# Performance work log

Hardware: AMD Instinct MI355X
Metric: run time of the kernel (lower is better)

The kernel has to match this reference:

```python
import jax, jax.numpy as jnp
import numpy as np

N, E, IN, H, D = 50000, 800000, 256, 4, 32
NEG_SLOPE = 0.2


def setup_inputs() -> dict:
    key = jax.random.key(0)
    ks = jax.random.split(key, 11)
    feat = jax.random.normal(ks[0], (N, IN), jnp.float32)
    src = jax.random.randint(ks[1], (E,), 0, N, jnp.int32)
    dst = jax.random.randint(ks[2], (E,), 0, N, jnp.int32)
    # ppmi in [1, 10) so log(log(ppmi)) path is non-trivial
    ppmi = 1.0 + 9.0 * jax.random.uniform(ks[3], (E,), jnp.float32)
    eps_src = jax.random.normal(ks[4], (N, H, 1), jnp.float32)
    eps_dst = jax.random.normal(ks[5], (N, H, 1), jnp.float32)
    W = jax.random.normal(ks[6], (IN, H * D), jnp.float32) * (1.0 / np.sqrt(IN))
    mu_src = jax.random.normal(ks[7], (1, H, D), jnp.float32) * 0.02
    mu_dst = jax.random.normal(ks[8], (1, H, D), jnp.float32) * 0.02
    lam_src = jax.random.normal(ks[9], (1, H, D), jnp.float32) * 0.02
    lam_dst = jax.random.normal(ks[10], (1, H, D), jnp.float32) * 0.02
    return dict(feat=feat, src=src, dst=dst, ppmi=ppmi, eps_src=eps_src,
                eps_dst=eps_dst, W=W, mu_src=mu_src, mu_dst=mu_dst,
                lam_src=lam_src, lam_dst=lam_dst)


def reference(feat, src, dst, ppmi, eps_src, eps_dst, W, mu_src, mu_dst, lam_src, lam_dst):
    n = feat.shape[0]
    h, d = mu_src.shape[1], mu_src.shape[2]
    ft = (feat @ W).reshape(n, h, d)                      # [N,H,D]
    # per-node attention scalars (src == dst node set here)
    mu_s = (ft * mu_src).sum(-1, keepdims=True)           # [N,H,1]
    lam_s = (ft * lam_src).sum(-1, keepdims=True)
    mu_d = (ft * mu_dst).sum(-1, keepdims=True)
    lam_d = (ft * lam_src).sum(-1, keepdims=True)         # original uses lam_src here (replicated)
    # reparameterize z = eps * exp(0.5*logvar) + mu
    z_src = eps_src * jnp.exp(0.5 * lam_s) + mu_s
    z_dst = eps_dst * jnp.exp(0.5 * lam_d) + mu_d
    e = jax.nn.leaky_relu(z_src[src] + z_dst[dst], NEG_SLOPE)   # [E,H,1]
    scale = jnp.clip(jnp.log(jnp.clip(jnp.log(ppmi), 1.0, None)), 1.0, None)
    e2 = e * scale[:, None, None]
    # edge softmax over destination segments
    emax = jax.ops.segment_max(e2, dst, num_segments=n)   # [N,H,1]
    ee = jnp.exp(e2 - emax[dst])
    denom = jax.ops.segment_sum(ee, dst, num_segments=n)
    a = ee / denom[dst]                                    # [E,H,1]
    # weighted scatter-sum aggregation: u_mul_e + sum
    rst = jax.ops.segment_sum(ft[src] * a, dst, num_segments=n)  # [N,H,D]
    return rst, mu_s + mu_d, lam_s + lam_d
```

## Files before the change

### kernel.cpp

```cpp
#include <hip/hip_runtime.h>

#define N_NODES 50000
#define N_EDGES 800000
#define IN_DIM  256
#define NH      4
#define HD      128
#define NEG_SLOPE 0.2f
#define SCAN_BLOCKS ((N_NODES + 255) / 256)
#define HIST_BLOCKS ((N_EDGES + 255) / 256)
#define WT_BLOCKS   ((HD * IN_DIM) / 256)
#define K1B_BLOCKS  ((N_NODES * NH + 255) / 256)

typedef short          v8s __attribute__((ext_vector_type(8)));
typedef float          v4f __attribute__((ext_vector_type(4)));
typedef unsigned short us8 __attribute__((ext_vector_type(8)));
typedef int            v4i __attribute__((ext_vector_type(4)));

__device__ __forceinline__ unsigned short f2bf(float f)
{
    unsigned int u = __float_as_uint(f);
    u += 0x7fffu + ((u >> 16) & 1u);
    return (unsigned short)(u >> 16);
}
__device__ __forceinline__ float bf2f(unsigned int bits16)
{
    return __uint_as_float(bits16 << 16);
}

__device__ __forceinline__ float edge_scale(float p)
{
    const float lp = fmaxf(__logf(p), 1.0f);
    return fmaxf(__logf(lp), 1.0f);
}

__global__ __launch_bounds__(256) void k_wt_hist(
    const float* __restrict__ W, unsigned short* __restrict__ Wt_bf,
    const int* __restrict__ dst, int* __restrict__ counts,
    int* __restrict__ rank)
{
    const int b = blockIdx.x;
    if (b < HIST_BLOCKS) {
        const int e = b * 256 + threadIdx.x;
        if (e < N_EDGES) rank[e] = atomicAdd(&counts[dst[e]], 1);
    } else {
        const int idx = (b - HIST_BLOCKS) * 256 + threadIdx.x;
        const int n = idx >> 8;
        const int k = idx & 255;
        Wt_bf[n * IN_DIM + k] = f2bf(W[(size_t)k * HD + n]);
    }
}

#define AS 40
#define CS 136

__global__ __launch_bounds__(256) void k1_mfma(
    const float* __restrict__ feat, const unsigned short* __restrict__ Wt_bf,
    unsigned short* __restrict__ ft_bf)
{
    __shared__ ushort smem[17408];
    ushort* A_sh = smem;
    ushort* B_sh = smem + 128 * AS;

    const int t    = threadIdx.x;
    const int lane = t & 63;
    const int wv   = t >> 6;
    const int r0   = blockIdx.x * 128;

    const int arow = t >> 3;
    const int akk  = (t & 7) * 4;
    int rA[4];
#pragma unroll
    for (int p = 0; p < 4; ++p) rA[p] = min(r0 + arow + 32 * p, N_NODES - 1);
    const int bn  = t >> 2;
    const int bk8 = (t & 3) * 8;

    float4 fa[4];
    us8    fb[2];

#define LOADC(kc0)                                                              \
    do {                                                                        \
        _Pragma("unroll")                                                       \
        for (int p = 0; p < 4; ++p)                                             \
            fa[p] = *(const float4*)(feat + (size_t)rA[p] * IN_DIM + (kc0) + akk); \
        _Pragma("unroll")                                                       \
        for (int p = 0; p < 2; ++p)                                             \
            fb[p] = *(const us8*)(Wt_bf + (size_t)(bn + 64 * p) * IN_DIM + (kc0) + bk8); \
    } while (0)

    v4f acc[2][8];
#pragma unroll
    for (int i = 0; i < 2; ++i)
#pragma unroll
        for (int j = 0; j < 8; ++j) acc[i][j] = (v4f)(0.0f);

    const int frow = lane & 15;
    const int fq   = lane >> 4;

    LOADC(0);

    for (int c = 0; c < IN_DIM / 32; ++c) {
        __syncthreads();
#pragma unroll
        for (int p = 0; p < 4; ++p) {
            ushort4 u;
            u.x = f2bf(fa[p].x); u.y = f2bf(fa[p].y);
            u.z = f2bf(fa[p].z); u.w = f2bf(fa[p].w);
            *(ushort4*)(A_sh + (arow + 32 * p) * AS + akk) = u;
        }
#pragma unroll
        for (int p = 0; p < 2; ++p)
            *(us8*)(B_sh + (bn + 64 * p) * AS + bk8) = fb[p];
        __syncthreads();

        if (c + 1 < IN_DIM / 32) LOADC((c + 1) * 32);

        v8s a0 = *(const v8s*)(A_sh + (wv * 32 + frow) * AS + fq * 8);
        v8s a1 = *(const v8s*)(A_sh + (wv * 32 + 16 + frow) * AS + fq * 8);
        v8s bfr[8];
#pragma unroll
        for (int nf = 0; nf < 8; ++nf)
            bfr[nf] = *(const v8s*)(B_sh + (nf * 16 + frow) * AS + fq * 8);
#pragma unroll
        for (int nf = 0; nf < 8; ++nf) {
            acc[0][nf] = __builtin_amdgcn_mfma_f32_16x16x32_bf16(
                a0, bfr[nf], acc[0][nf], 0, 0, 0);
            acc[1][nf] = __builtin_amdgcn_mfma_f32_16x16x32_bf16(
                a1, bfr[nf], acc[1][nf], 0, 0, 0);
        }
    }

    __syncthreads();
    ushort* Cw = smem + wv * (32 * CS);
#pragma unroll
    for (int mf = 0; mf < 2; ++mf)
#pragma unroll
        for (int nf = 0; nf < 8; ++nf)
#pragma unroll
            for (int r = 0; r < 4; ++r)
                Cw[(mf * 16 + fq * 4 + r) * CS + nf * 16 + frow] =
                    f2bf(acc[mf][nf][r]);
    __syncthreads();

#pragma unroll
    for (int p = 0; p < 8; ++p) {
        const int row_l = (lane >> 4) + 4 * p;
        const int colv  = (lane & 15) * 8;
        const us8 val = *(const us8*)(Cw + row_l * CS + colv);
        const int grow = r0 + wv * 32 + row_l;
        if (grow < N_NODES)
            *(us8*)(ft_bf + (size_t)grow * HD + colv) = val;
    }
}

__global__ __launch_bounds__(256) void k_k1b_scanlocal(
    const int* __restrict__ counts, int* __restrict__ local,
    int* __restrict__ bsums,
    const unsigned short* __restrict__ ft_bf,
    const float* __restrict__ mu_src, const float* __restrict__ mu_dst,
    const float* __restrict__ lam_src,
    const float* __restrict__ eps_src, const float* __restrict__ eps_dst,
    float* __restrict__ z_src_ws, float* __restrict__ z_dst_ws,
    float* __restrict__ mu_out, float* __restrict__ lam_out)
{
    __shared__ int sh[256];
    const int b = blockIdx.x;
    const int t = threadIdx.x;

    if (b < SCAN_BLOCKS) {
        const int i = b * 256 + t;
        const int v = (i < N_NODES) ? counts[i] : 0;
        sh[t] = v;
        __syncthreads();
#pragma unroll
        for (int off = 1; off < 256; off <<= 1) {
            int x = (t >= off) ? sh[t - off] : 0;
            __syncthreads();
            sh[t] += x;
            __syncthreads();
        }
        if (i < N_NODES) local[i] = sh[t] - v;
        if (t == 255) bsums[b] = sh[255];
        return;
    }

    const int g = (b - SCAN_BLOCKS) * 256 + t;
    if (g >= N_NODES * NH) return;
    const int row = g >> 2;
    const int h   = g & 3;

    const unsigned short* fr = ft_bf + (size_t)row * HD + h * 32;
    const float* ms = mu_src + h * 32;
    const float* md = mu_dst + h * 32;
    const float* ls = lam_src + h * 32;

    float pm = 0.0f, pd = 0.0f, pl = 0.0f;
#pragma unroll
    for (int v = 0; v < 4; ++v) {
        const us8 u = *(const us8*)(fr + v * 8);
#pragma unroll
        for (int j = 0; j < 8; ++j) {
            const float f = bf2f(u[j]);
            const int   i = v * 8 + j;
            pm = fmaf(f, ms[i], pm);
            pd = fmaf(f, md[i], pd);
            pl = fmaf(f, ls[i], pl);
        }
    }
    const float sdev = expf(0.5f * pl);
    z_src_ws[g] = eps_src[g] * sdev + pm;
    z_dst_ws[g] = eps_dst[g] * sdev + pd;
    mu_out[g]   = pm + pd;
    lam_out[g]  = 2.0f * pl;
}

__global__ __launch_bounds__(256) void k_scan_bsums(
    const int* __restrict__ bsums, int* __restrict__ bscan)
{
    __shared__ int sh[256];
    const int t = threadIdx.x;
    const int v = (t < SCAN_BLOCKS) ? bsums[t] : 0;
    sh[t] = v;
    __syncthreads();
#pragma unroll
    for (int off = 1; off < 256; off <<= 1) {
        int x = (t >= off) ? sh[t - off] : 0;
        __syncthreads();
        sh[t] += x;
        __syncthreads();
    }
    if (t < SCAN_BLOCKS) bscan[t] = sh[t] - v;
}

__global__ __launch_bounds__(256) void k_scan_add(
    const int* __restrict__ local, const int* __restrict__ bscan,
    int* __restrict__ offsets)
{
    const int i = blockIdx.x * 256 + threadIdx.x;
    if (i >= N_NODES) return;
    offsets[i] = local[i] + bscan[blockIdx.x];
}

__global__ __launch_bounds__(256) void k_scatter(
    const int* __restrict__ src, const int* __restrict__ dst,
    const float* __restrict__ ppmi, const int* __restrict__ rank,
    const int* __restrict__ offsets, v4i* __restrict__ rec_sorted)
{
    const int e = blockIdx.x * 256 + threadIdx.x;
    if (e >= N_EDGES) return;
    const int d0 = dst[e];
    const int j  = offsets[d0] + rank[e];
    v4i rec;
    rec.x = src[e];
    rec.y = __float_as_int(edge_scale(ppmi[e]));
    rec.z = 0;
    rec.w = 0;
    __builtin_nontemporal_store(rec, rec_sorted + j);
}

__device__ __forceinline__ float edge_w1(float zs, float zd, float sc)
{
    float v = zs + zd;
    v = (v >= 0.0f) ? v : NEG_SLOPE * v;
    return __expf(v * sc);
}

__global__ __launch_bounds__(64) void k3_csr(
    const int* __restrict__ offsets, const int* __restrict__ counts,
    const v4i* __restrict__ rec_sorted,
    const float* __restrict__ z_src_ws, const float* __restrict__ z_dst_ws,
    const uint4* __restrict__ ft_u128, float2* __restrict__ rst2)
{
    const int node = blockIdx.x;
    const int lane = threadIdx.x;
    const int es   = lane >> 4;
    const int li   = lane & 15;
    const int h    = li >> 2;
    const int start = offsets[node];
    const int deg   = counts[node];
    const float zd  = z_dst_ws[node * NH + h];

    float acc[8] = {0, 0, 0, 0, 0, 0, 0, 0};
    float wsum = 0.0f;

#define K3_EDGE(EI)                                                            \
    do {                                                                       \
        const int  ei  = (EI);                                                 \
        const int  idx = start + ((ei < deg) ? ei : 0);                        \
        const v4i  r   = __builtin_nontemporal_load(rec_sorted + idx);         \
        const float zs = z_src_ws[r.x * NH + h];                               \
        const uint4 f  = ft_u128[(size_t)r.x * 16 + li];                       \
        float w = edge_w1(zs, zd, __int_as_float(r.y));                        \
        if (ei >= deg) w = 0.0f;                                               \
        acc[0] = fmaf(bf2f(f.x & 0xffffu), w, acc[0]);                         \
        acc[1] = fmaf(bf2f(f.x >> 16),     w, acc[1]);                         \
        acc[2] = fmaf(bf2f(f.y & 0xffffu), w, acc[2]);                         \
        acc[3] = fmaf(bf2f(f.y >> 16),     w, acc[3]);                         \
        acc[4] = fmaf(bf2f(f.z & 0xffffu), w, acc[4]);                         \
        acc[5] = fmaf(bf2f(f.z >> 16),     w, acc[5]);                         \
        acc[6] = fmaf(bf2f(f.w & 0xffffu), w, acc[6]);                         \
        acc[7] = fmaf(bf2f(f.w >> 16),     w, acc[7]);                         \
        wsum += w;                                                             \
    } while (0)

    int i = 0;
    for (; i + 8 <= deg; i += 8) {
        K3_EDGE(i + es);
        K3_EDGE(i + 4 + es);
    }
    if (i < deg) K3_EDGE(i + es);
    if (i + 4 < deg) K3_EDGE(i + 4 + es);

#pragma unroll
    for (int m = 16; m <= 32; m <<= 1) {
        wsum += __shfl_xor(wsum, m, 64);
#pragma unroll
        for (int j = 0; j < 8; ++j) acc[j] += __shfl_xor(acc[j], m, 64);
    }

    const float inv = (wsum > 0.0f) ? 1.0f / wsum : 0.0f;
    rst2[(size_t)node * 64 + li * 4 + es] =
        make_float2(acc[es * 2] * inv, acc[es * 2 + 1] * inv);
}

extern "C" void kernel_launch(void* const* d_in, const int* in_sizes, int n_in,
                              void* d_out, int out_size, void* d_ws, size_t ws_size,
                              hipStream_t stream)
{
    const float* feat    = (const float*)d_in[0];
    const int*   src     = (const int*)  d_in[1];
    const int*   dst     = (const int*)  d_in[2];
    const float* ppmi    = (const float*)d_in[3];
    const float* eps_src = (const float*)d_in[4];
    const float* eps_dst = (const float*)d_in[5];
    const float* W       = (const float*)d_in[6];
    const float* mu_src  = (const float*)d_in[7];
    const float* mu_dst  = (const float*)d_in[8];
    const float* lam_src = (const float*)d_in[9];

    float* out     = (float*)d_out;
    float* rst     = out;
    float* mu_out  = out + (size_t)N_NODES * HD;
    float* lam_out = mu_out + (size_t)N_NODES * NH;

    char* wsb = (char*)d_ws;
    v4i*            rec_s  = (v4i*)wsb;
    unsigned short* ft_bf  = (unsigned short*)(wsb + (size_t)N_EDGES * 16);
    unsigned short* Wt_bf  = ft_bf + (size_t)N_NODES * HD;
    float*          zs_ws  = (float*)(Wt_bf + (size_t)HD * IN_DIM);
    float*          zd_ws  = zs_ws + (size_t)N_NODES * NH;
    int*            counts = (int*)(zd_ws + (size_t)N_NODES * NH);
    int*            local  = counts + N_NODES;
    int*            offsets= local + N_NODES;
    int*            bsums  = offsets + N_NODES;
    int*            bscan  = bsums + 256;
    int*            rank   = bscan + 256;

    hipMemsetAsync(counts, 0, N_NODES * sizeof(int), stream);

    k_wt_hist<<<HIST_BLOCKS + WT_BLOCKS, 256, 0, stream>>>(
        W, Wt_bf, dst, counts, rank);

    k1_mfma<<<(N_NODES + 127) / 128, 256, 0, stream>>>(feat, Wt_bf, ft_bf);

    k_k1b_scanlocal<<<SCAN_BLOCKS + K1B_BLOCKS, 256, 0, stream>>>(
        counts, local, bsums,
        ft_bf, mu_src, mu_dst, lam_src, eps_src, eps_dst,
        zs_ws, zd_ws, mu_out, lam_out);

    k_scan_bsums<<<1, 256, 0, stream>>>(bsums, bscan);
    k_scan_add<<<SCAN_BLOCKS, 256, 0, stream>>>(local, bscan, offsets);

    k_scatter<<<HIST_BLOCKS, 256, 0, stream>>>(
        src, dst, ppmi, rank, offsets, rec_s);

    k3_csr<<<N_NODES, 64, 0, stream>>>(
        offsets, counts, rec_s, zs_ws, zd_ws,
        (const uint4*)ft_bf, (float2*)rst);
}
```

Before: 240.7 us.

## Shrink edge records to 8 bytes and pack four nodes per aggregation block

Edge records written by the scatter and read by the CSR aggregation kernel are cut from 16 to 8 bytes by dropping two unused padding ints. The aggregation kernel now runs four nodes per 256-thread block instead of one node per 64-thread block, unrolls the edge loop to 16 edges per iteration with a single masked tail, and writes the output with nontemporal stores. The aim is to lower record traffic, reduce per-block launch overhead and expose more memory-level parallelism. The larger unroll adds masked dummy loads for low-degree nodes.

New measurement: 236.4 us. Within noise of the previous version (-1.8%).

```diff
diff --git a/kernel.cpp b/kernel.cpp
--- a/kernel.cpp
+++ b/kernel.cpp
@@ -13,8 +13,9 @@
 
 typedef short          v8s __attribute__((ext_vector_type(8)));
 typedef float          v4f __attribute__((ext_vector_type(4)));
+typedef float          v2f __attribute__((ext_vector_type(2)));
 typedef unsigned short us8 __attribute__((ext_vector_type(8)));
-typedef int            v4i __attribute__((ext_vector_type(4)));
+typedef int            v2i __attribute__((ext_vector_type(2)));
 
 __device__ __forceinline__ unsigned short f2bf(float f)
 {
@@ -243,17 +244,15 @@
 __global__ __launch_bounds__(256) void k_scatter(
     const int* __restrict__ src, const int* __restrict__ dst,
     const float* __restrict__ ppmi, const int* __restrict__ rank,
-    const int* __restrict__ offsets, v4i* __restrict__ rec_sorted)
+    const int* __restrict__ offsets, v2i* __restrict__ rec_sorted)
 {
     const int e = blockIdx.x * 256 + threadIdx.x;
     if (e >= N_EDGES) return;
     const int d0 = dst[e];
     const int j  = offsets[d0] + rank[e];
-    v4i rec;
+    v2i rec;
     rec.x = src[e];
     rec.y = __float_as_int(edge_scale(ppmi[e]));
-    rec.z = 0;
-    rec.w = 0;
     __builtin_nontemporal_store(rec, rec_sorted + j);
 }
 
@@ -264,14 +263,14 @@
     return __expf(v * sc);
 }
 
-__global__ __launch_bounds__(64) void k3_csr(
+__global__ __launch_bounds__(256, 8) void k3_csr(
     const int* __restrict__ offsets, const int* __restrict__ counts,
-    const v4i* __restrict__ rec_sorted,
+    const v2i* __restrict__ rec_sorted,
     const float* __restrict__ z_src_ws, const float* __restrict__ z_dst_ws,
-    const uint4* __restrict__ ft_u128, float2* __restrict__ rst2)
-{
-    const int node = blockIdx.x;
-    const int lane = threadIdx.x;
+    const uint4* __restrict__ ft_u128, v2f* __restrict__ rst2)
+{
+    const int node = blockIdx.x * 4 + (threadIdx.x >> 6);
+    const int lane = threadIdx.x & 63;
     const int es   = lane >> 4;
     const int li   = lane & 15;
     const int h    = li >> 2;
@@ -286,7 +285,7 @@
     do {                                                                       \
         const int  ei  = (EI);                                                 \
         const int  idx = start + ((ei < deg) ? ei : 0);                        \
-        const v4i  r   = __builtin_nontemporal_load(rec_sorted + idx);         \
+        const v2i  r   = __builtin_nontemporal_load(rec_sorted + idx);         \
         const float zs = z_src_ws[r.x * NH + h];                               \
         const uint4 f  = ft_u128[(size_t)r.x * 16 + li];                       \
         float w = edge_w1(zs, zd, __int_as_float(r.y));                        \
@@ -303,12 +302,18 @@
     } while (0)
 
     int i = 0;
-    for (; i + 8 <= deg; i += 8) {
+    for (; i + 16 <= deg; i += 16) {
         K3_EDGE(i + es);
         K3_EDGE(i + 4 + es);
-    }
-    if (i < deg) K3_EDGE(i + es);
-    if (i + 4 < deg) K3_EDGE(i + 4 + es);
+        K3_EDGE(i + 8 + es);
+        K3_EDGE(i + 12 + es);
+    }
+    if (i < deg) {
+        K3_EDGE(i + es);
+        K3_EDGE(i + 4 + es);
+        K3_EDGE(i + 8 + es);
+        K3_EDGE(i + 12 + es);
+    }
 
 #pragma unroll
     for (int m = 16; m <= 32; m <<= 1) {
@@ -318,8 +323,10 @@
     }
 
     const float inv = (wsum > 0.0f) ? 1.0f / wsum : 0.0f;
-    rst2[(size_t)node * 64 + li * 4 + es] =
-        make_float2(acc[es * 2] * inv, acc[es * 2 + 1] * inv);
+    v2f o;
+    o.x = acc[es * 2] * inv;
+    o.y = acc[es * 2 + 1] * inv;
+    __builtin_nontemporal_store(o, &rst2[(size_t)node * 64 + li * 4 + es]);
 }
 
 extern "C" void kernel_launch(void* const* d_in, const int* in_sizes, int n_in,
@@ -343,8 +350,8 @@
     float* lam_out = mu_out + (size_t)N_NODES * NH;
 
     char* wsb = (char*)d_ws;
-    v4i*            rec_s  = (v4i*)wsb;
-    unsigned short* ft_bf  = (unsigned short*)(wsb + (size_t)N_EDGES * 16);
+    v2i*            rec_s  = (v2i*)wsb;
+    unsigned short* ft_bf  = (unsigned short*)(wsb + (size_t)N_EDGES * 8);
     unsigned short* Wt_bf  = ft_bf + (size_t)N_NODES * HD;
     float*          zs_ws  = (float*)(Wt_bf + (size_t)HD * IN_DIM);
     float*          zd_ws  = zs_ws + (size_t)N_NODES * NH;
@@ -373,7 +380,7 @@
     k_scatter<<<HIST_BLOCKS, 256, 0, stream>>>(
         src, dst, ppmi, rank, offsets, rec_s);
 
-    k3_csr<<<N_NODES, 64, 0, stream>>>(
+    k3_csr<<<N_NODES / 4, 256, 0, stream>>>(
         offsets, counts, rec_s, zs_ws, zd_ws,
-        (const uint4*)ft_bf, (float2*)rst);
-}
+        (const uint4*)ft_bf, (v2f*)rst);
+}
```
